# Optimization experiments

Measured on AMD Instinct MI355X. Metric: run time of the kernel, lower is better.

The kernel has to match this reference:

```python
import jax, jax.numpy as jnp
import numpy as np

B, M, N = 16384, 512, 2048
N_ITERS = 10


def setup_inputs() -> dict:
    key = jax.random.key(0)
    kb, kD = jax.random.split(key)
    batch = jax.random.normal(kb, (B, M), dtype=jnp.float32)
    # nn.Parameter(torch.rand((M, N))) -> uniform [0,1)
    D = jax.random.uniform(kD, (M, N), dtype=jnp.float32)
    gamma = jnp.float32(0.1)
    beta = jnp.float32(0.1)
    return {"batch": batch, "D": D, "gamma": gamma, "beta": beta}


def reference(batch, D, gamma, beta):
    # Vectorized AMP sparse coding: the original loops over batch items; here
    # the per-sample matvecs D.T@v and D@alpha become batched GEMMs v@D, a@D.T.
    y = batch                                   # [B, M]
    m = D.shape[0]
    sqrt_m = jnp.sqrt(jnp.asarray(m, y.dtype))
    alpha0 = jnp.zeros((y.shape[0], D.shape[1]), dtype=y.dtype)  # [B, N]

    def amp_step(carry, _):
        alpha, v = carry
        z = alpha + beta * (v @ D)                               # [B, N]
        # per-sample threshold t = gamma/sqrt(M) * ||v||_2
        t = (gamma / sqrt_m) * jnp.linalg.norm(v, axis=-1, keepdims=True)  # [B,1]
        new_alpha = jnp.maximum(z - t, 0.0) * jnp.sign(z)        # relu(z-t)*sign(z)
        new_v = (y - beta * (new_alpha @ D.T)
                 + (beta / m) * jnp.linalg.norm(new_alpha, axis=-1, keepdims=True) * v)
        return (new_alpha, new_v), None

    (alpha, _v), _ = jax.lax.scan(amp_step, (alpha0, y), None, length=N_ITERS)
    return alpha
```

## Files before the change

### kernel.cpp

```cpp
#include <hip/hip_runtime.h>
#include <math.h>

#define Bsz 16384
#define Msz 512
#define Nsz 2048

typedef _Float16 half8 __attribute__((ext_vector_type(8)));
typedef _Float16 half4 __attribute__((ext_vector_type(4)));
typedef _Float16 half2v __attribute__((ext_vector_type(2)));
typedef float floatx16 __attribute__((ext_vector_type(16)));
typedef unsigned int uint;

struct HL { _Float16 h, l; };
__device__ __forceinline__ HL split1(float x) {
    HL r;
    r.h = (_Float16)x;
    r.l = (_Float16)(x - (float)r.h);
    return r;
}
__device__ __forceinline__ uint packHL(float x) {
    HL s = split1(x);
    return (uint)__builtin_bit_cast(unsigned short, s.h)
         | ((uint)__builtin_bit_cast(unsigned short, s.l) << 16);
}
__device__ __forceinline__ float unpackHL(uint w) {
    half2v p = __builtin_bit_cast(half2v, w);
    return (float)p.x + (float)p.y;
}

__device__ __forceinline__ void gl_lds16(const _Float16* g, _Float16* l) {
    __builtin_amdgcn_global_load_lds(
        (const __attribute__((address_space(1))) unsigned int*)g,
        (__attribute__((address_space(3))) unsigned int*)l, 16, 0, 0);
}

#define BAR()  asm volatile("s_barrier" ::: "memory")


__global__ __launch_bounds__(256) void zero_kernel(float4* __restrict__ p) {
    p[blockIdx.x * 256 + threadIdx.x] = make_float4(0.f, 0.f, 0.f, 0.f);
}

__global__ __launch_bounds__(256) void init_kernel(const float* __restrict__ batch,
        _Float16* __restrict__ vh, float* __restrict__ t2) {
    const int wave = threadIdx.x >> 6;
    const int lane = threadIdx.x & 63;
    const int b = (blockIdx.x << 2) + wave;
    const float* row = batch + (size_t)b * Msz + lane * 8;
    float4 a = *(const float4*)row;
    float4 c = *(const float4*)(row + 4);
    half8 h;
    h[0] = (_Float16)a.x; h[1] = (_Float16)a.y;
    h[2] = (_Float16)a.z; h[3] = (_Float16)a.w;
    h[4] = (_Float16)c.x; h[5] = (_Float16)c.y;
    h[6] = (_Float16)c.z; h[7] = (_Float16)c.w;
    const size_t off = ((size_t)(b >> 5) * 32 + (lane >> 1)) * 512
                     + ((size_t)(lane & 1) << 8) + ((b & 31) << 3);
    *(half8*)(vh + off) = h;
    float s = a.x*a.x + a.y*a.y + a.z*a.z + a.w*a.w
            + c.x*c.x + c.y*c.y + c.z*c.z + c.w*c.w;
#pragma unroll
    for (int off2 = 32; off2 > 0; off2 >>= 1) s += __shfl_down(s, off2);
    if (lane == 0) t2[b] = s;
}

__global__ __launch_bounds__(256) void convD_kernel(const float* __restrict__ D,
        _Float16* __restrict__ Dph, _Float16* __restrict__ Dtph) {
    __shared__ float T[64][65];
    const int t = threadIdx.x;
    const int tx = t & 15, ty = t >> 4;
    const int n0 = blockIdx.x << 6, m0 = blockIdx.y << 6;
#pragma unroll
    for (int q = 0; q < 4; ++q) {
        const int mr = m0 + (ty << 2) + q;
        const int nc = n0 + (tx << 2);
        float4 d = *(const float4*)(D + (size_t)mr * Nsz + nc);
        half4 h;
        h[0] = (_Float16)d.x; h[1] = (_Float16)d.y;
        h[2] = (_Float16)d.z; h[3] = (_Float16)d.w;
        const size_t o2 = ((size_t)(mr >> 5) * 128 + (nc >> 4)) * 512
                        + (((size_t)(nc >> 3) & 1) << 8) + ((mr & 31) << 3) + (nc & 7);
        *(half4*)(Dph + o2) = h;
        T[(tx << 2) + 0][(ty << 2) + q] = d.x;
        T[(tx << 2) + 1][(ty << 2) + q] = d.y;
        T[(tx << 2) + 2][(ty << 2) + q] = d.z;
        T[(tx << 2) + 3][(ty << 2) + q] = d.w;
    }
    __syncthreads();
#pragma unroll
    for (int q = 0; q < 4; ++q) {
        const int nr = n0 + (ty << 2) + q;
        const int mc = m0 + (tx << 2);
        float4 d = make_float4(T[(ty << 2) + q][tx << 2],
                               T[(ty << 2) + q][(tx << 2) + 1],
                               T[(ty << 2) + q][(tx << 2) + 2],
                               T[(ty << 2) + q][(tx << 2) + 3]);
        half4 h;
        h[0] = (_Float16)d.x; h[1] = (_Float16)d.y;
        h[2] = (_Float16)d.z; h[3] = (_Float16)d.w;
        const size_t o1 = ((size_t)(nr >> 5) * 32 + (mc >> 4)) * 512
                        + (((size_t)(mc >> 3) & 1) << 8) + ((nr & 31) << 3) + (mc & 7);
        *(half4*)(Dtph + o1) = h;
    }
}

template<int FIRST, int LAST>
__global__ __launch_bounds__(256, 4) void gemm1_kernel(
        const _Float16* __restrict__ Av,
        const _Float16* __restrict__ Bth,
        const float* __restrict__ t2,
        uint* __restrict__ alphaP,
        float* __restrict__ na2,
        const float* __restrict__ beta_p, const float* __restrict__ gamma_p) {
    const int tid = threadIdx.x;
    const int wave = tid >> 6, lane = tid & 63;
    const int wy = wave >> 1, wx = wave & 1;
    const int ln = lane & 31, lh = lane >> 5;
    const int bid = blockIdx.x;
    const int b0 = (bid & 127) << 7;
    const int n0 = (bid >> 7) << 7;
    const int R0 = b0 >> 5, C0 = n0 >> 5;

    floatx16 acc[2][2] = {};

    const _Float16* pa0 = Av  + ((size_t)(R0 + 2 * wy)     * 32) * 512 + lane * 8;
    const _Float16* pa1 = Av  + ((size_t)(R0 + 2 * wy + 1) * 32) * 512 + lane * 8;
    const _Float16* pb0 = Bth + ((size_t)(C0 + 2 * wx)     * 32) * 512 + lane * 8;
    const _Float16* pb1 = Bth + ((size_t)(C0 + 2 * wx + 1) * 32) * 512 + lane * 8;

    half8 xa0, xa1, xb0, xb1;
    half8 ya0, ya1, yb0, yb1;

    xa0 = *(const half8*)(pa0);
    xa1 = *(const half8*)(pa1);
    xb0 = *(const half8*)(pb0);
    xb1 = *(const half8*)(pb1);

    for (int kt = 0; kt < 32; kt += 2) {
        {
            const size_t o = (size_t)(kt + 1) << 9;
            ya0 = *(const half8*)(pa0 + o);
            ya1 = *(const half8*)(pa1 + o);
            yb0 = *(const half8*)(pb0 + o);
            yb1 = *(const half8*)(pb1 + o);
            acc[0][0] = __builtin_amdgcn_mfma_f32_32x32x16_f16(xa0, xb0, acc[0][0], 0, 0, 0);
            acc[1][0] = __builtin_amdgcn_mfma_f32_32x32x16_f16(xa1, xb0, acc[1][0], 0, 0, 0);
            acc[0][1] = __builtin_amdgcn_mfma_f32_32x32x16_f16(xa0, xb1, acc[0][1], 0, 0, 0);
            acc[1][1] = __builtin_amdgcn_mfma_f32_32x32x16_f16(xa1, xb1, acc[1][1], 0, 0, 0);
        }
        {
            if (kt + 2 < 32) {
                const size_t o = (size_t)(kt + 2) << 9;
                xa0 = *(const half8*)(pa0 + o);
                xa1 = *(const half8*)(pa1 + o);
                xb0 = *(const half8*)(pb0 + o);
                xb1 = *(const half8*)(pb1 + o);
            }
            acc[0][0] = __builtin_amdgcn_mfma_f32_32x32x16_f16(ya0, yb0, acc[0][0], 0, 0, 0);
            acc[1][0] = __builtin_amdgcn_mfma_f32_32x32x16_f16(ya1, yb0, acc[1][0], 0, 0, 0);
            acc[0][1] = __builtin_amdgcn_mfma_f32_32x32x16_f16(ya0, yb1, acc[0][1], 0, 0, 0);
            acc[1][1] = __builtin_amdgcn_mfma_f32_32x32x16_f16(ya1, yb1, acc[1][1], 0, 0, 0);
        }
    }

    const float beta = beta_p[0];
    const float tc = gamma_p[0] * 0.044194173824159216f;
#pragma unroll
    for (int i = 0; i < 2; ++i) {
#pragma unroll
        for (int reg = 0; reg < 16; ++reg) {
            const int rr = (reg & 3) + 8 * (reg >> 2) + 4 * lh;
            const int b = b0 + wy * 64 + i * 32 + rr;
            const float tb2 = tc * sqrtf(t2[b]);
            uint* arow = alphaP + (size_t)b * Nsz + n0 + wx * 64 + ln;
            float s = 0.f;
#pragma unroll
            for (int j = 0; j < 2; ++j) {
                float z = FIRST ? 0.f : unpackHL(arow[j * 32]);
                float val = fmaxf(fmaf(beta, acc[i][j][reg], z) - tb2, 0.f);
                if (LAST) ((float*)arow)[j * 32] = val;
                else      arow[j * 32] = packHL(val);
                s = fmaf(val, val, s);
            }
            s += __shfl_down(s, 16, 32);
            s += __shfl_down(s, 8, 32);
            s += __shfl_down(s, 4, 32);
            s += __shfl_down(s, 2, 32);
            s += __shfl_down(s, 1, 32);
            if (ln == 0) atomicAdd(&na2[b], s);
        }
    }
}

__global__ __launch_bounds__(256, 2) void gemm2_kernel(
        const uint* __restrict__ alphaP,
        const _Float16* __restrict__ Bh,
        const float* __restrict__ na2,
        const float* __restrict__ y,
        _Float16* __restrict__ vh,
        float* __restrict__ t2,
        const float* __restrict__ beta_p) {
    __shared__ _Float16 lds[16384];

    const int tid = threadIdx.x;
    const int wave = tid >> 6, lane = tid & 63;
    const int wy = wave >> 1, wx = wave & 1;
    const int ln = lane & 31, lh = lane >> 5;
    const int bid = blockIdx.x;
    const int b0 = (bid & 127) << 7;
    const int m0 = (bid >> 7) << 7;
    const int C0 = m0 >> 5;

    floatx16 acc[2][2] = {};

    const int srow = tid >> 1;
    const int skq  = (tid & 1) << 4;
    const uint* apP = alphaP + (size_t)(b0 + srow) * Nsz + skq;
    const int awo = ((((srow >> 5) << 1) + (skq >> 4)) << 9) + ((srow & 31) << 3);

    const _Float16* gB = Bh + ((size_t)(C0 + wave) * 128) * 512 + lane * 8;
    const int fB = 8 + wave * 2;

    const int ro = lane << 3;

    uint4 a0, a1, a2, a3;
    auto loadA = [&](int c) {
        const uint* nx = apP + c * 32;
        a0 = *(const uint4*)(nx);
        a1 = *(const uint4*)(nx + 4);
        a2 = *(const uint4*)(nx + 8);
        a3 = *(const uint4*)(nx + 12);
    };
    auto writeA = [&](int d) {
        uint4 ha, hb;
        ha.x = __builtin_amdgcn_perm(a0.y, a0.x, 0x05040100u);
        ha.y = __builtin_amdgcn_perm(a0.w, a0.z, 0x05040100u);
        ha.z = __builtin_amdgcn_perm(a1.y, a1.x, 0x05040100u);
        ha.w = __builtin_amdgcn_perm(a1.w, a1.z, 0x05040100u);
        hb.x = __builtin_amdgcn_perm(a2.y, a2.x, 0x05040100u);
        hb.y = __builtin_amdgcn_perm(a2.w, a2.z, 0x05040100u);
        hb.z = __builtin_amdgcn_perm(a3.y, a3.x, 0x05040100u);
        hb.w = __builtin_amdgcn_perm(a3.w, a3.z, 0x05040100u);
        _Float16* aw = lds + d * 8192 + awo;
        *(uint4*)aw = ha;
        *(uint4*)(aw + 256) = hb;
    };
    auto stageB = [&](int c, int d) {
        _Float16* lB = lds + d * 8192;
#pragma unroll
        for (int kt = 0; kt < 2; ++kt)
            gl_lds16(gB + (size_t)kt * 512 + (size_t)c * 1024, lB + ((fB + kt) << 9));
    };

    loadA(0);
    writeA(0);
    stageB(0, 0);
    loadA(1);
    writeA(1);
    stageB(1, 1);
    loadA(2);
    asm volatile("s_waitcnt vmcnt(6) lgkmcnt(0)" ::: "memory");
    BAR();

    for (int c = 0; c < 64; ++c) {
        const _Float16* lb = lds + (c & 1) * 8192;
        __builtin_amdgcn_s_setprio(1);
#pragma unroll
        for (int ks = 0; ks < 2; ++ks) {
            half8 fa[2], fb[2];
#pragma unroll
            for (int i = 0; i < 2; ++i) {
                fa[i] = *(const half8*)(lb + ((((wy * 2 + i) << 1) + ks) << 9) + ro);
                fb[i] = *(const half8*)(lb + 4096 + ((((wx * 2 + i) << 1) + ks) << 9) + ro);
            }
#pragma unroll
            for (int j = 0; j < 2; ++j)
#pragma unroll
                for (int i = 0; i < 2; ++i)
                    acc[i][j] = __builtin_amdgcn_mfma_f32_32x32x16_f16(fa[i], fb[j], acc[i][j], 0, 0, 0);
        }
        __builtin_amdgcn_s_setprio(0);
        if (c == 63) break;
        BAR();
        if (c < 61) {
            stageB(c + 2, c & 1);
            writeA(c & 1);
            loadA(c + 3);
            asm volatile("s_waitcnt vmcnt(6) lgkmcnt(0)" ::: "memory");
        } else if (c == 61) {
            stageB(63, 1);
            writeA(1);
            asm volatile("s_waitcnt vmcnt(2) lgkmcnt(0)" ::: "memory");
        } else {
            asm volatile("s_waitcnt vmcnt(0) lgkmcnt(0)" ::: "memory");
        }
        BAR();
    }

    const float beta = beta_p[0];
#pragma unroll
    for (int i = 0; i < 2; ++i) {
#pragma unroll
        for (int reg = 0; reg < 16; ++reg) {
            const int rr = (reg & 3) + 8 * (reg >> 2) + 4 * lh;
            const int b = b0 + wy * 64 + i * 32 + rr;
            const float cb = beta * (1.0f / 512.0f) * sqrtf(na2[b]);
            float s = 0.f;
#pragma unroll
            for (int j = 0; j < 2; ++j) {
                const int m = m0 + wx * 64 + j * 32 + ln;
                const size_t po = ((size_t)(b >> 5) * 32 + (m >> 4)) * 512
                                + (((size_t)(m >> 3) & 1) << 8) + ((b & 31) << 3) + (m & 7);
                const size_t yi = (size_t)b * Msz + m;
                float vold = (float)vh[po];
                float val = y[yi] - beta * acc[i][j][reg] + cb * vold;
                vh[po] = (_Float16)val;
                s = fmaf(val, val, s);
            }
            s += __shfl_down(s, 16, 32);
            s += __shfl_down(s, 8, 32);
            s += __shfl_down(s, 4, 32);
            s += __shfl_down(s, 2, 32);
            s += __shfl_down(s, 1, 32);
            if (ln == 0) atomicAdd(&t2[b], s);
        }
    }
}

extern "C" void kernel_launch(void* const* d_in, const int* in_sizes, int n_in,
                              void* d_out, int out_size, void* d_ws, size_t ws_size,
                              hipStream_t stream) {
    (void)in_sizes; (void)n_in; (void)out_size; (void)ws_size;
    const float* batch   = (const float*)d_in[0];
    const float* D       = (const float*)d_in[1];
    const float* gamma_p = (const float*)d_in[2];
    const float* beta_p  = (const float*)d_in[3];

    uint* alphaP = (uint*)d_out;

    _Float16* vh   = (_Float16*)d_ws;
    _Float16* Dph  = vh + (size_t)Bsz * Msz;
    _Float16* Dtph = Dph + (size_t)Msz * Nsz;
    float*    t2s  = (float*)(Dtph + (size_t)Msz * Nsz);
    float*    na2s = t2s + 10 * Bsz;

    zero_kernel<<<19 * Bsz / 1024, 256, 0, stream>>>((float4*)(t2s + Bsz));
    convD_kernel<<<dim3(Nsz / 64, Msz / 64), 256, 0, stream>>>(D, Dph, Dtph);
    init_kernel<<<Bsz / 4, 256, 0, stream>>>(batch, vh, t2s);

    for (int it = 0; it < 10; ++it) {
        if (it == 0)
            gemm1_kernel<1, 0><<<2048, 256, 0, stream>>>(vh, Dtph,
                    t2s + (size_t)it * Bsz, alphaP, na2s + (size_t)it * Bsz,
                    beta_p, gamma_p);
        else if (it == 9)
            gemm1_kernel<0, 1><<<2048, 256, 0, stream>>>(vh, Dtph,
                    t2s + (size_t)it * Bsz, alphaP, na2s + (size_t)it * Bsz,
                    beta_p, gamma_p);
        else
            gemm1_kernel<0, 0><<<2048, 256, 0, stream>>>(vh, Dtph,
                    t2s + (size_t)it * Bsz, alphaP, na2s + (size_t)it * Bsz,
                    beta_p, gamma_p);
        if (it < 9) {
            gemm2_kernel<<<512, 256, 0, stream>>>(alphaP, Dph,
                                                  na2s + (size_t)it * Bsz,
                                                  batch, vh,
                                                  t2s + (size_t)(it + 1) * Bsz,
                                                  beta_p);
        }
    }
}
```

Measured before the change: 1.650 ms.

## Load gemm2 B fragments directly from global into registers instead of LDS

In gemm2, the B operand (Bh) tiles are no longer staged into LDS through global_load_lds. Each wave now reads its own B fragments straight from global memory into registers, double-buffered across k-halves, and LDS holds only the A tile. This halves LDS use, which may raise occupancy, and drops one barrier per iteration. In exchange, B fragments shared by waves with the same wx are loaded twice from global or L2, and the pipeline depth for A and B prefetch is shortened.

After: 1.682 ms. Within noise of the previous version (+2.0%).

```diff
diff --git a/kernel.cpp b/kernel.cpp
--- a/kernel.cpp
+++ b/kernel.cpp
@@ -26,12 +26,6 @@
 __device__ __forceinline__ float unpackHL(uint w) {
     half2v p = __builtin_bit_cast(half2v, w);
     return (float)p.x + (float)p.y;
-}
-
-__device__ __forceinline__ void gl_lds16(const _Float16* g, _Float16* l) {
-    __builtin_amdgcn_global_load_lds(
-        (const __attribute__((address_space(1))) unsigned int*)g,
-        (__attribute__((address_space(3))) unsigned int*)l, 16, 0, 0);
 }
 
 #define BAR()  asm volatile("s_barrier" ::: "memory")
@@ -200,7 +194,7 @@
         _Float16* __restrict__ vh,
         float* __restrict__ t2,
         const float* __restrict__ beta_p) {
-    __shared__ _Float16 lds[16384];
+    __shared__ _Float16 lds[8192];
 
     const int tid = threadIdx.x;
     const int wave = tid >> 6, lane = tid & 63;
@@ -218,8 +212,8 @@
     const uint* apP = alphaP + (size_t)(b0 + srow) * Nsz + skq;
     const int awo = ((((srow >> 5) << 1) + (skq >> 4)) << 9) + ((srow & 31) << 3);
 
-    const _Float16* gB = Bh + ((size_t)(C0 + wave) * 128) * 512 + lane * 8;
-    const int fB = 8 + wave * 2;
+    const _Float16* pb0 = Bh + ((size_t)(C0 + 2 * wx)     * 128) * 512 + lane * 8;
+    const _Float16* pb1 = Bh + ((size_t)(C0 + 2 * wx + 1) * 128) * 512 + lane * 8;
 
     const int ro = lane << 3;
 
@@ -241,59 +235,51 @@
         hb.y = __builtin_amdgcn_perm(a2.w, a2.z, 0x05040100u);
         hb.z = __builtin_amdgcn_perm(a3.y, a3.x, 0x05040100u);
         hb.w = __builtin_amdgcn_perm(a3.w, a3.z, 0x05040100u);
-        _Float16* aw = lds + d * 8192 + awo;
+        _Float16* aw = lds + d * 4096 + awo;
         *(uint4*)aw = ha;
         *(uint4*)(aw + 256) = hb;
     };
-    auto stageB = [&](int c, int d) {
-        _Float16* lB = lds + d * 8192;
-#pragma unroll
-        for (int kt = 0; kt < 2; ++kt)
-            gl_lds16(gB + (size_t)kt * 512 + (size_t)c * 1024, lB + ((fB + kt) << 9));
-    };
+
+    half8 xb0, xb1, yb0, yb1;
 
     loadA(0);
     writeA(0);
-    stageB(0, 0);
     loadA(1);
-    writeA(1);
-    stageB(1, 1);
-    loadA(2);
-    asm volatile("s_waitcnt vmcnt(6) lgkmcnt(0)" ::: "memory");
+    xb0 = *(const half8*)(pb0);
+    xb1 = *(const half8*)(pb1);
+    asm volatile("s_waitcnt lgkmcnt(0)" ::: "memory");
     BAR();
 
     for (int c = 0; c < 64; ++c) {
-        const _Float16* lb = lds + (c & 1) * 8192;
-        __builtin_amdgcn_s_setprio(1);
-#pragma unroll
-        for (int ks = 0; ks < 2; ++ks) {
-            half8 fa[2], fb[2];
-#pragma unroll
-            for (int i = 0; i < 2; ++i) {
-                fa[i] = *(const half8*)(lb + ((((wy * 2 + i) << 1) + ks) << 9) + ro);
-                fb[i] = *(const half8*)(lb + 4096 + ((((wx * 2 + i) << 1) + ks) << 9) + ro);
+        const _Float16* lb = lds + (c & 1) * 4096;
+        {
+            const size_t o = ((size_t)(2 * c + 1)) << 9;
+            yb0 = *(const half8*)(pb0 + o);
+            yb1 = *(const half8*)(pb1 + o);
+            half8 fa0 = *(const half8*)(lb + ((((wy * 2 + 0) << 1) + 0) << 9) + ro);
+            half8 fa1 = *(const half8*)(lb + ((((wy * 2 + 1) << 1) + 0) << 9) + ro);
+            acc[0][0] = __builtin_amdgcn_mfma_f32_32x32x16_f16(fa0, xb0, acc[0][0], 0, 0, 0);
+            acc[1][0] = __builtin_amdgcn_mfma_f32_32x32x16_f16(fa1, xb0, acc[1][0], 0, 0, 0);
+            acc[0][1] = __builtin_amdgcn_mfma_f32_32x32x16_f16(fa0, xb1, acc[0][1], 0, 0, 0);
+            acc[1][1] = __builtin_amdgcn_mfma_f32_32x32x16_f16(fa1, xb1, acc[1][1], 0, 0, 0);
+        }
+        {
+            if (c < 63) {
+                const size_t o = ((size_t)(2 * c + 2)) << 9;
+                xb0 = *(const half8*)(pb0 + o);
+                xb1 = *(const half8*)(pb1 + o);
             }
-#pragma unroll
-            for (int j = 0; j < 2; ++j)
-#pragma unroll
-                for (int i = 0; i < 2; ++i)
-                    acc[i][j] = __builtin_amdgcn_mfma_f32_32x32x16_f16(fa[i], fb[j], acc[i][j], 0, 0, 0);
-        }
-        __builtin_amdgcn_s_setprio(0);
+            half8 fa0 = *(const half8*)(lb + ((((wy * 2 + 0) << 1) + 1) << 9) + ro);
+            half8 fa1 = *(const half8*)(lb + ((((wy * 2 + 1) << 1) + 1) << 9) + ro);
+            acc[0][0] = __builtin_amdgcn_mfma_f32_32x32x16_f16(fa0, yb0, acc[0][0], 0, 0, 0);
+            acc[1][0] = __builtin_amdgcn_mfma_f32_32x32x16_f16(fa1, yb0, acc[1][0], 0, 0, 0);
+            acc[0][1] = __builtin_amdgcn_mfma_f32_32x32x16_f16(fa0, yb1, acc[0][1], 0, 0, 0);
+            acc[1][1] = __builtin_amdgcn_mfma_f32_32x32x16_f16(fa1, yb1, acc[1][1], 0, 0, 0);
+        }
         if (c == 63) break;
-        BAR();
-        if (c < 61) {
-            stageB(c + 2, c & 1);
-            writeA(c & 1);
-            loadA(c + 3);
-            asm volatile("s_waitcnt vmcnt(6) lgkmcnt(0)" ::: "memory");
-        } else if (c == 61) {
-            stageB(63, 1);
-            writeA(1);
-            asm volatile("s_waitcnt vmcnt(2) lgkmcnt(0)" ::: "memory");
-        } else {
-            asm volatile("s_waitcnt vmcnt(0) lgkmcnt(0)" ::: "memory");
-        }
+        writeA((c + 1) & 1);
+        if (c < 62) loadA(c + 2);
+        asm volatile("s_waitcnt lgkmcnt(0)" ::: "memory");
         BAR();
     }
 
```
